# Kernel tuning notes

Hardware: AMD Instinct MI355X
Metric: run time of the kernel (lower is better)

## Reference

```python
import jax, jax.numpy as jnp
import numpy as np

B, S, D, H = 32, 8192, 128, 256  # batch-of-MLPs, seq_len, emb_dim, hidden_dim
LN_EPS = 1e-5


def setup_inputs() -> dict:
    key = jax.random.key(0)
    k0, k1, k2, k3 = jax.random.split(key, 4)
    x = jax.random.normal(k0, (B, S, D), dtype=jnp.float32)
    # shared learned Q projection (torch Linear stores W as [out,in]; y = x @ W.T)
    Wq = jax.random.normal(k1, (D, D), dtype=jnp.float32) / np.float32(np.sqrt(D))
    # per-batch-index (non-shared) fast-weight MLP params
    W1 = jax.random.normal(k2, (B, D, H), dtype=jnp.float32) / np.float32(np.sqrt(D))
    b1 = jnp.zeros((B, H), dtype=jnp.float32)
    W2 = jax.random.normal(k3, (B, H, D), dtype=jnp.float32) / np.float32(np.sqrt(H))
    b2 = jnp.zeros((B, D), dtype=jnp.float32)
    gamma = jnp.ones((B, D), dtype=jnp.float32)
    beta = jnp.zeros((B, D), dtype=jnp.float32)
    return dict(x=x, Wq=Wq, W1=W1, b1=b1, W2=W2, b2=b2, gamma=gamma, beta=beta)


def reference(x, Wq, W1, b1, W2, b2, gamma, beta):
    # queries = silu(Q(x))
    q = jax.nn.silu(jnp.einsum('bsd,ed->bse', x, Wq))
    # torch F.normalize with default dim=1 -> L2-normalize over the sequence axis
    q = q / jnp.clip(jnp.linalg.norm(q, axis=1, keepdims=True), 1e-12)
    # ParallelMLPs: per-index MLP with distinct weights (grouped GEMM), + residual
    h = jax.nn.silu(jnp.einsum('bsd,bdh->bsh', q, W1) + b1[:, None, :])
    o = jnp.einsum('bsh,bhd->bsd', h, W2) + b2[:, None, :]
    mu = jnp.mean(o, axis=-1, keepdims=True)
    var = jnp.mean(jnp.square(o - mu), axis=-1, keepdims=True)
    ln = (o - mu) / jnp.sqrt(var + LN_EPS) * gamma[:, None, :] + beta[:, None, :]
    return ln + q
```

## Files before the change

kernel.cpp:

```cpp
#include <hip/hip_runtime.h>
#include <stdint.h>

#define B_ 32
#define S_ 8192
#define D_ 128
#define H_ 256

typedef __attribute__((ext_vector_type(4))) float f32x4;
typedef __attribute__((ext_vector_type(16))) float f32x16;
typedef __attribute__((ext_vector_type(8))) short bf16x8;
typedef __attribute__((ext_vector_type(4))) unsigned int u32x4;

__device__ __forceinline__ unsigned short f2bf(float f) {
    union { float f; unsigned int u; } v; v.f = f;
    unsigned int r = v.u + 0x7fffu + ((v.u >> 16) & 1u);
    return (unsigned short)(r >> 16);
}
__device__ __forceinline__ float bf2f(unsigned short u) {
    union { unsigned int u; float f; } v; v.u = ((unsigned int)u) << 16;
    return v.f;
}
__device__ __forceinline__ float silu_f(float v) {
    return v * __builtin_amdgcn_rcpf(1.0f + __expf(-v));
}
__device__ __forceinline__ unsigned int cvtpk(float lo, float hi) {
    unsigned int r;
    asm("v_cvt_pk_bf16_f32 %0, %1, %2" : "=v"(r) : "v"(lo), "v"(hi));
    return r;
}
__device__ __forceinline__ void plswap(unsigned int& a, unsigned int& b) {
    asm("v_permlane32_swap_b32 %0, %1" : "+v"(a), "+v"(b));
}
__device__ __forceinline__ void gl16(const void* g, void* l) {
    __builtin_amdgcn_global_load_lds(
        (const __attribute__((address_space(1))) unsigned int*)g,
        (__attribute__((address_space(3))) unsigned int*)l, 16, 0, 0);
}

__global__ void k_prep(const float* __restrict__ Wq, const float* __restrict__ W1,
                       const float* __restrict__ W2, const float* __restrict__ b1,
                       unsigned short* __restrict__ wq_bf,
                       unsigned short* __restrict__ w1s,
                       unsigned short* __restrict__ w2s,
                       float* __restrict__ b1r) {
    __shared__ __align__(16) unsigned short tile[8192];
    int t = threadIdx.x, blk = blockIdx.x;
    if (blk < 128) {
        int b = blk >> 2, hc = blk & 3;
#pragma unroll
        for (int i = 0; i < 8; i++) {
            int idx = t + i * 256;
            int d = idx >> 4, hj = idx & 15;
            f32x4 v = *(const f32x4*)(W1 + ((size_t)(b * D_ + d)) * H_ + hc * 64 + hj * 4);
#pragma unroll
            for (int u = 0; u < 4; u++) tile[(hj * 4 + u) * 128 + d] = f2bf(v[u]);
        }
        __syncthreads();
        char* img = (char*)w1s + (size_t)blk * 16384;
#pragma unroll
        for (int i = 0; i < 4; i++) {
            int c = t + i * 256;
            int n = c >> 9, kk = (c >> 6) & 7, l = c & 63;
            u32x4 v = *(const u32x4*)(tile + (n * 32 + (l & 31)) * 128 + kk * 16 + (l >> 5) * 8);
            *(u32x4*)(img + c * 16) = v;
        }
    } else if (blk < 256) {
        int a = blk - 128;
        int b = a >> 2, hc = a & 3;
#pragma unroll
        for (int i = 0; i < 8; i++) {
            int idx = t + i * 256;
            int h = idx >> 5, d4 = idx & 31;
            f32x4 v = *(const f32x4*)(W2 + ((size_t)(b * H_ + hc * 64 + h)) * D_ + d4 * 4);
#pragma unroll
            for (int u = 0; u < 4; u++) tile[(d4 * 4 + u) * 64 + h] = f2bf(v[u]);
        }
        __syncthreads();
        char* img = (char*)w2s + (size_t)a * 16384;
#pragma unroll
        for (int i = 0; i < 4; i++) {
            int c = t + i * 256;
            int dn = c >> 8, n = (c >> 7) & 1, kk2 = (c >> 6) & 1, l = c & 63;
            u32x4 v = *(const u32x4*)(tile + (dn * 32 + (l & 31)) * 64 + n * 32 + kk2 * 16 + (l >> 5) * 8);
            *(u32x4*)(img + c * 16) = v;
        }
    } else if (blk < 320) {
        int i = (blk - 256) * 256 + t;
        wq_bf[i] = f2bf(Wq[i]);
    } else {
        int idx = (blk - 320) * 256 + t;
        int b = idx >> 8, rem = idx & 255;
        int hc = rem >> 6, n = (rem >> 5) & 1, hi = (rem >> 4) & 1, r = rem & 15;
        int h = hc * 64 + n * 32 + (r & 3) + 8 * (r >> 2) + 4 * hi;
        b1r[idx] = b1[b * H_ + h];
    }
}

__global__ __launch_bounds__(256, 2) void k_qproj(
        const float* __restrict__ x, const unsigned short* __restrict__ wq_bf,
        unsigned short* __restrict__ q_img, float* __restrict__ part) {
    __shared__ __align__(16) unsigned short lds_a[128 * 128];
    __shared__ __align__(16) unsigned short lds_b[128 * 128];
    __shared__ float lds_ss[4][128];

    int tid = threadIdx.x;
    int lane = tid & 63, w = tid >> 6;
    int g = lane >> 4, c15 = lane & 15;
    int blk = blockIdx.x;
    int b = blk >> 6, st = blk & 63;
    size_t rowbase = (size_t)b * S_ + (size_t)st * 128;
    const float* xg = x + rowbase * D_;

    char* pA = (char*)lds_a;
    char* pB = (char*)lds_b;

#pragma unroll
    for (int i = 0; i < 8; i++) {
        int idx = tid + i * 256;
        int row = idx >> 4, cb = idx & 15;
        u32x4 v = *(const u32x4*)(wq_bf + row * 128 + cb * 8);
        *(u32x4*)(pB + row * 256 + (((unsigned)cb ^ (unsigned)(row & 7)) << 4)) = v;
    }
#pragma unroll
    for (int i = 0; i < 16; i++) {
        int idx = tid + i * 256;
        int row = idx >> 5, c4 = idx & 31;
        f32x4 v = *(const f32x4*)(xg + (size_t)row * 128 + c4 * 4);
        unsigned int lo = cvtpk(v[0], v[1]), hi2 = cvtpk(v[2], v[3]);
        *(unsigned long long*)(pA + row * 256 + ((c4 * 8) ^ ((row & 7) << 4))) =
            ((unsigned long long)hi2 << 32) | (unsigned long long)lo;
    }
    __syncthreads();

    f32x4 acc[2][8];
#pragma unroll
    for (int m = 0; m < 2; m++)
#pragma unroll
        for (int n = 0; n < 8; n++) acc[m][n] = (f32x4)0.0f;

#pragma unroll
    for (int kk = 0; kk < 4; kk++) {
        int kb = kk * 64 + (g << 4);
        bf16x8 a[2];
#pragma unroll
        for (int m = 0; m < 2; m++) {
            int row = (w << 5) + (m << 4) + c15;
            a[m] = *(const bf16x8*)(pA + row * 256 + (kb ^ ((row & 7) << 4)));
        }
#pragma unroll
        for (int n = 0; n < 8; n++) {
            int rowb = (n << 4) + c15;
            bf16x8 bb = *(const bf16x8*)(pB + rowb * 256 + (kb ^ ((rowb & 7) << 4)));
#pragma unroll
            for (int m = 0; m < 2; m++)
                acc[m][n] = __builtin_amdgcn_mfma_f32_16x16x32_bf16(a[m], bb, acc[m][n], 0, 0, 0);
        }
    }

    float ss[8];
#pragma unroll
    for (int n = 0; n < 8; n++) ss[n] = 0.0f;
#pragma unroll
    for (int m = 0; m < 2; m++)
#pragma unroll
        for (int n = 0; n < 8; n++)
#pragma unroll
            for (int r = 0; r < 4; r++) {
                float v = silu_f(acc[m][n][r]);
                acc[m][n][r] = v;
                ss[n] += v * v;
            }
#pragma unroll
    for (int n = 0; n < 8; n++) {
        float v = ss[n];
        v += __shfl_xor(v, 16, 64);
        v += __shfl_xor(v, 32, 64);
        if (lane < 16) lds_ss[w][(n << 4) + lane] = v;
    }
    __syncthreads();

#pragma unroll
    for (int m = 0; m < 2; m++)
#pragma unroll
        for (int n = 0; n < 8; n++)
#pragma unroll
            for (int r = 0; r < 4; r++) {
                int row = (w << 5) + (m << 4) + (g << 2) + r;
                int col = (n << 4) + c15;
                int byte = (row >> 5) * 8192 + (col >> 4) * 1024 +
                           ((row & 31) + ((col >> 3) & 1) * 32) * 16 + (col & 7) * 2;
                *(unsigned short*)(pA + byte) = f2bf(acc[m][n][r]);
            }
    __syncthreads();

    char* qo = (char*)q_img + ((size_t)(b * 256 + st * 4)) * 8192;
#pragma unroll
    for (int i = 0; i < 8; i++) {
        int off = tid * 16 + i * 4096;
        *(u32x4*)(qo + off) = *(const u32x4*)(pA + off);
    }
    if (tid < 128) {
        float s = lds_ss[0][tid] + lds_ss[1][tid] + lds_ss[2][tid] + lds_ss[3][tid];
        part[((size_t)b * 64 + st) * 128 + tid] = s;
    }
}

__global__ void k_scale(const float* __restrict__ part, float* __restrict__ scale) {
    int idx = blockIdx.x * 256 + threadIdx.x;
    int b = idx >> 7, e = idx & 127;
    const float* p = part + (size_t)b * 64 * 128 + e;
    float s = 0.0f;
    for (int t = 0; t < 64; t++) s += p[t * 128];
    scale[idx] = 1.0f / fmaxf(sqrtf(s), 1e-12f);
}

__global__ void k_wscale(unsigned short* __restrict__ w1s, const float* __restrict__ scale) {
    int blk = blockIdx.x;
    int b = blk >> 2;
    char* region = (char*)w1s + (size_t)blk * 16384;
    int t = threadIdx.x;
#pragma unroll
    for (int i = 0; i < 4; i++) {
        int c = t + i * 256;
        int kk = (c >> 6) & 7, l = c & 63;
        int d0 = kk * 16 + (l >> 5) * 8;
        u32x4 v = *(const u32x4*)(region + c * 16);
        const unsigned short* pv = (const unsigned short*)&v;
        const float* sc = scale + b * D_ + d0;
        u32x4 o;
#pragma unroll
        for (int j = 0; j < 4; j++)
            o[j] = cvtpk(bf2f(pv[2 * j]) * sc[2 * j], bf2f(pv[2 * j + 1]) * sc[2 * j + 1]);
        *(u32x4*)(region + c * 16) = o;
    }
}

__global__ __launch_bounds__(512, 4) void k_mlp(
        const unsigned short* __restrict__ q_img, const float* __restrict__ scale,
        const unsigned short* __restrict__ w1s, const unsigned short* __restrict__ w2s,
        const float* __restrict__ b1r, const float* __restrict__ b2,
        const float* __restrict__ gamma, const float* __restrict__ beta,
        float* __restrict__ out) {
    __shared__ __align__(16) char lds[65536];
    int tid = threadIdx.x;
    int lane = tid & 63, w = tid >> 6;
    int c31 = lane & 31, hi = lane >> 5;
    int blk = blockIdx.x;
    int b = blk >> 5, st2 = blk & 31;

    const char* w1b = (const char*)w1s + (size_t)(b * 4) * 16384;
    const char* w2b = (const char*)w2s + (size_t)(b * 4) * 16384;
    size_t grp = (size_t)(b * 256 + st2 * 8 + w);
    const char* qg = (const char*)q_img + grp * 8192;

#define STAGE(bufoff, hcn) do {                                               \
    _Pragma("unroll")                                                          \
    for (int i_ = 0; i_ < 2; i_++) {                                           \
        int off_ = w * 2048 + i_ * 1024;                                       \
        gl16(w1b + (hcn) * 16384 + off_ + lane * 16, lds + (bufoff) + off_);   \
        gl16(w2b + (hcn) * 16384 + off_ + lane * 16, lds + (bufoff) + 16384 + off_); \
    } } while (0)

    STAGE(0, 0);

    bf16x8 qf[8];
#pragma unroll
    for (int kk = 0; kk < 8; kk++)
        qf[kk] = *(const bf16x8*)(qg + kk * 1024 + lane * 16);

    float scv[4], gv[4], bev[4];
    f32x16 acco[4];
#pragma unroll
    for (int dn = 0; dn < 4; dn++) {
        int d = dn * 32 + c31;
        scv[dn] = scale[b * 128 + d];
        gv[dn]  = gamma[b * 128 + d];
        bev[dn] = beta[b * 128 + d];
        float bb = b2[b * 128 + d];
#pragma unroll
        for (int e = 0; e < 16; e++) acco[dn][e] = bb;
    }

    __syncthreads();

#pragma unroll
    for (int hc = 0; hc < 4; hc++) {
        int buf = (hc & 1) * 32768;
        if (hc < 3) STAGE(buf ^ 32768, hc + 1);

        bf16x8 pa[2][2];
#pragma unroll
        for (int n = 0; n < 2; n++) {
            const float* b1p = b1r + ((b * 4 + hc) * 2 + n) * 32 + hi * 16;
            f32x16 acch;
#pragma unroll
            for (int jq = 0; jq < 4; jq++) {
                f32x4 bq = *(const f32x4*)(b1p + jq * 4);
#pragma unroll
                for (int e = 0; e < 4; e++) acch[jq * 4 + e] = bq[e];
            }
#pragma unroll
            for (int kk = 0; kk < 8; kk++) {
                bf16x8 wf = *(const bf16x8*)(lds + buf + n * 8192 + kk * 1024 + lane * 16);
                acch = __builtin_amdgcn_mfma_f32_32x32x16_bf16(wf, qf[kk], acch, 0, 0, 0);
            }
            float sv[16];
#pragma unroll
            for (int r = 0; r < 16; r++) sv[r] = silu_f(acch[r]);
            unsigned int P[8];
#pragma unroll
            for (int p = 0; p < 8; p++) P[p] = cvtpk(sv[2 * p], sv[2 * p + 1]);
            plswap(P[0], P[2]); plswap(P[1], P[3]);
            plswap(P[4], P[6]); plswap(P[5], P[7]);
            union { unsigned int u[4]; bf16x8 v; } f0, f1;
            f0.u[0] = P[0]; f0.u[1] = P[1]; f0.u[2] = P[2]; f0.u[3] = P[3];
            f1.u[0] = P[4]; f1.u[1] = P[5]; f1.u[2] = P[6]; f1.u[3] = P[7];
            pa[n][0] = f0.v; pa[n][1] = f1.v;
        }

#pragma unroll
        for (int dn = 0; dn < 4; dn++)
#pragma unroll
            for (int n = 0; n < 2; n++)
#pragma unroll
                for (int kk2 = 0; kk2 < 2; kk2++) {
                    bf16x8 wf2 = *(const bf16x8*)(lds + buf + 16384 + dn * 4096 +
                                                  n * 2048 + kk2 * 1024 + lane * 16);
                    acco[dn] = __builtin_amdgcn_mfma_f32_32x32x16_bf16(pa[n][kk2], wf2, acco[dn], 0, 0, 0);
                }

        if (hc < 3) __syncthreads();
    }
#undef STAGE

    __syncthreads();
    char* myq = (char*)lds + w * 8192;
#pragma unroll
    for (int kk = 0; kk < 8; kk++)
        *(bf16x8*)(myq + c31 * 256 + ((kk * 32 + hi * 16) ^ ((c31 & 7) << 4))) = qf[kk];

    float* og = out + grp * 32 * 128;
#pragma unroll
    for (int r = 0; r < 16; r++) {
        float v0 = acco[0][r], v1 = acco[1][r], v2 = acco[2][r], v3 = acco[3][r];
        float s1 = (v0 + v1) + (v2 + v3);
        float s2 = (v0 * v0 + v1 * v1) + (v2 * v2 + v3 * v3);
        s1 += __shfl_xor(s1, 1, 64);   s2 += __shfl_xor(s2, 1, 64);
        s1 += __shfl_xor(s1, 2, 64);   s2 += __shfl_xor(s2, 2, 64);
        s1 += __shfl_xor(s1, 4, 64);   s2 += __shfl_xor(s2, 4, 64);
        s1 += __shfl_xor(s1, 8, 64);   s2 += __shfl_xor(s2, 8, 64);
        s1 += __shfl_xor(s1, 16, 64);  s2 += __shfl_xor(s2, 16, 64);
        float mu = s1 * (1.0f / 128.0f);
        float var = s2 * (1.0f / 128.0f) - mu * mu;
        float rstd = rsqrtf(var + 1e-5f);
        int srow0 = (r & 3) + 8 * (r >> 2);
        int row = srow0 + 4 * hi;
#pragma unroll
        for (int dn = 0; dn < 4; dn++) {
            float qv = bf2f(*(const unsigned short*)(myq + row * 256 +
                        ((dn * 64 + c31 * 2) ^ ((row & 7) << 4)))) * scv[dn];
            float o = (acco[dn][r] - mu) * rstd * gv[dn] + bev[dn] + qv;
            og[(size_t)row * 128 + dn * 32 + c31] = o;
        }
    }
}

extern "C" void kernel_launch(void* const* d_in, const int* in_sizes, int n_in,
                              void* d_out, int out_size, void* d_ws, size_t ws_size,
                              hipStream_t stream) {
    (void)in_sizes; (void)n_in; (void)out_size; (void)ws_size;
    const float* x     = (const float*)d_in[0];
    const float* Wq    = (const float*)d_in[1];
    const float* W1    = (const float*)d_in[2];
    const float* b1    = (const float*)d_in[3];
    const float* W2    = (const float*)d_in[4];
    const float* b2    = (const float*)d_in[5];
    const float* gamma = (const float*)d_in[6];
    const float* beta  = (const float*)d_in[7];
    float* out = (float*)d_out;

    char* ws = (char*)d_ws;
    unsigned short* wq_bf = (unsigned short*)(ws);
    unsigned short* w1s   = (unsigned short*)(ws + 32768);
    unsigned short* w2s   = (unsigned short*)(ws + 2129920);
    float* part           = (float*)(ws + 4227072);
    float* scale          = (float*)(ws + 5275648);
    float* b1r            = (float*)(ws + 5292032);
    unsigned short* q_img = (unsigned short*)(ws + 5324800);

    hipLaunchKernelGGL(k_prep, dim3(352), dim3(256), 0, stream, Wq, W1, W2, b1, wq_bf, w1s, w2s, b1r);
    hipLaunchKernelGGL(k_qproj, dim3(2048), dim3(256), 0, stream, x, wq_bf, q_img, part);
    hipLaunchKernelGGL(k_scale, dim3(16), dim3(256), 0, stream, part, scale);
    hipLaunchKernelGGL(k_wscale, dim3(128), dim3(256), 0, stream, w1s, scale);
    hipLaunchKernelGGL(k_mlp, dim3(1024), dim3(512), 0, stream,
                       q_img, scale, w1s, w2s, b1r, b2, gamma, beta, out);
}
```

Before: 153.6 us.

## Halve MLP block size and LDS, single-buffer weights to raise occupancy

The fused MLP kernel now runs 256-thread blocks (4 waves) over twice as many blocks and uses a single 32 KB LDS weight buffer instead of a double-buffered 64 KB one. Launch bounds move to 5 blocks per SM, and the hc loop is no longer unrolled. The b2 bias and the gamma/beta/scale loads are deferred to the epilogue to cut live registers. The aim is higher occupancy so that other waves hide latency, at the cost of losing the prefetch overlap: each stage now sits between two barriers, and each block reloads the weights.

```diff
diff --git a/kernel.cpp b/kernel.cpp
--- a/kernel.cpp
+++ b/kernel.cpp
@@ -235,59 +235,49 @@
     }
 }
 
-__global__ __launch_bounds__(512, 4) void k_mlp(
+__global__ __launch_bounds__(256, 5) void k_mlp(
         const unsigned short* __restrict__ q_img, const float* __restrict__ scale,
         const unsigned short* __restrict__ w1s, const unsigned short* __restrict__ w2s,
         const float* __restrict__ b1r, const float* __restrict__ b2,
         const float* __restrict__ gamma, const float* __restrict__ beta,
         float* __restrict__ out) {
-    __shared__ __align__(16) char lds[65536];
+    __shared__ __align__(16) char lds[32768];
     int tid = threadIdx.x;
     int lane = tid & 63, w = tid >> 6;
     int c31 = lane & 31, hi = lane >> 5;
     int blk = blockIdx.x;
-    int b = blk >> 5, st2 = blk & 31;
+    int b = blk >> 6, st = blk & 63;
 
     const char* w1b = (const char*)w1s + (size_t)(b * 4) * 16384;
     const char* w2b = (const char*)w2s + (size_t)(b * 4) * 16384;
-    size_t grp = (size_t)(b * 256 + st2 * 8 + w);
+    size_t grp = (size_t)(b * 256 + st * 4 + w);
     const char* qg = (const char*)q_img + grp * 8192;
 
-#define STAGE(bufoff, hcn) do {                                               \
+#define STAGE(hcn) do {                                                        \
     _Pragma("unroll")                                                          \
-    for (int i_ = 0; i_ < 2; i_++) {                                           \
-        int off_ = w * 2048 + i_ * 1024;                                       \
-        gl16(w1b + (hcn) * 16384 + off_ + lane * 16, lds + (bufoff) + off_);   \
-        gl16(w2b + (hcn) * 16384 + off_ + lane * 16, lds + (bufoff) + 16384 + off_); \
+    for (int i_ = 0; i_ < 4; i_++) {                                           \
+        int off_ = w * 1024 + i_ * 4096;                                       \
+        gl16(w1b + (hcn) * 16384 + off_ + lane * 16, lds + off_);              \
+        gl16(w2b + (hcn) * 16384 + off_ + lane * 16, lds + 16384 + off_);      \
     } } while (0)
 
-    STAGE(0, 0);
+    STAGE(0);
 
     bf16x8 qf[8];
 #pragma unroll
     for (int kk = 0; kk < 8; kk++)
         qf[kk] = *(const bf16x8*)(qg + kk * 1024 + lane * 16);
 
-    float scv[4], gv[4], bev[4];
     f32x16 acco[4];
 #pragma unroll
-    for (int dn = 0; dn < 4; dn++) {
-        int d = dn * 32 + c31;
-        scv[dn] = scale[b * 128 + d];
-        gv[dn]  = gamma[b * 128 + d];
-        bev[dn] = beta[b * 128 + d];
-        float bb = b2[b * 128 + d];
-#pragma unroll
-        for (int e = 0; e < 16; e++) acco[dn][e] = bb;
-    }
+    for (int dn = 0; dn < 4; dn++)
+#pragma unroll
+        for (int e = 0; e < 16; e++) acco[dn][e] = 0.0f;
 
     __syncthreads();
 
-#pragma unroll
+#pragma unroll 1
     for (int hc = 0; hc < 4; hc++) {
-        int buf = (hc & 1) * 32768;
-        if (hc < 3) STAGE(buf ^ 32768, hc + 1);
-
         bf16x8 pa[2][2];
 #pragma unroll
         for (int n = 0; n < 2; n++) {
@@ -301,7 +291,7 @@
             }
 #pragma unroll
             for (int kk = 0; kk < 8; kk++) {
-                bf16x8 wf = *(const bf16x8*)(lds + buf + n * 8192 + kk * 1024 + lane * 16);
+                bf16x8 wf = *(const bf16x8*)(lds + n * 8192 + kk * 1024 + lane * 16);
                 acch = __builtin_amdgcn_mfma_f32_32x32x16_bf16(wf, qf[kk], acch, 0, 0, 0);
             }
             float sv[16];
@@ -324,12 +314,16 @@
             for (int n = 0; n < 2; n++)
 #pragma unroll
                 for (int kk2 = 0; kk2 < 2; kk2++) {
-                    bf16x8 wf2 = *(const bf16x8*)(lds + buf + 16384 + dn * 4096 +
+                    bf16x8 wf2 = *(const bf16x8*)(lds + 16384 + dn * 4096 +
                                                   n * 2048 + kk2 * 1024 + lane * 16);
                     acco[dn] = __builtin_amdgcn_mfma_f32_32x32x16_bf16(pa[n][kk2], wf2, acco[dn], 0, 0, 0);
                 }
 
-        if (hc < 3) __syncthreads();
+        if (hc < 3) {
+            __syncthreads();
+            STAGE(hc + 1);
+            __syncthreads();
+        }
     }
 #undef STAGE
 
@@ -339,10 +333,21 @@
     for (int kk = 0; kk < 8; kk++)
         *(bf16x8*)(myq + c31 * 256 + ((kk * 32 + hi * 16) ^ ((c31 & 7) << 4))) = qf[kk];
 
+    float scv[4], gv[4], bev[4], b2v[4];
+#pragma unroll
+    for (int dn = 0; dn < 4; dn++) {
+        int d = dn * 32 + c31;
+        scv[dn] = scale[b * 128 + d];
+        gv[dn]  = gamma[b * 128 + d];
+        bev[dn] = beta[b * 128 + d];
+        b2v[dn] = b2[b * 128 + d];
+    }
+
     float* og = out + grp * 32 * 128;
 #pragma unroll
     for (int r = 0; r < 16; r++) {
-        float v0 = acco[0][r], v1 = acco[1][r], v2 = acco[2][r], v3 = acco[3][r];
+        float v0 = acco[0][r] + b2v[0], v1 = acco[1][r] + b2v[1];
+        float v2 = acco[2][r] + b2v[2], v3 = acco[3][r] + b2v[3];
         float s1 = (v0 + v1) + (v2 + v3);
         float s2 = (v0 * v0 + v1 * v1) + (v2 * v2 + v3 * v3);
         s1 += __shfl_xor(s1, 1, 64);   s2 += __shfl_xor(s2, 1, 64);
@@ -355,11 +360,12 @@
         float rstd = rsqrtf(var + 1e-5f);
         int srow0 = (r & 3) + 8 * (r >> 2);
         int row = srow0 + 4 * hi;
+        float vv[4] = {v0, v1, v2, v3};
 #pragma unroll
         for (int dn = 0; dn < 4; dn++) {
             float qv = bf2f(*(const unsigned short*)(myq + row * 256 +
                         ((dn * 64 + c31 * 2) ^ ((row & 7) << 4)))) * scv[dn];
-            float o = (acco[dn][r] - mu) * rstd * gv[dn] + bev[dn] + qv;
+            float o = (vv[dn] - mu) * rstd * gv[dn] + bev[dn] + qv;
             og[(size_t)row * 128 + dn * 32 + c31] = o;
         }
     }
@@ -392,6 +398,6 @@
     hipLaunchKernelGGL(k_qproj, dim3(2048), dim3(256), 0, stream, x, wq_bf, q_img, part);
     hipLaunchKernelGGL(k_scale, dim3(16), dim3(256), 0, stream, part, scale);
     hipLaunchKernelGGL(k_wscale, dim3(128), dim3(256), 0, stream, w1s, scale);
-    hipLaunchKernelGGL(k_mlp, dim3(1024), dim3(512), 0, stream,
+    hipLaunchKernelGGL(k_mlp, dim3(2048), dim3(256), 0, stream,
                        q_img, scale, w1s, w2s, b1r, b2, gamma, beta, out);
 }
```

Measured after the change: 408.6 us. 166% more time.
